# Kernel optimization log

Hardware: AMD Instinct MI355X
Metric: run time of the kernel (lower is better)

The kernel has to match this reference:

```python
import jax, jax.numpy as jnp
import numpy as np

NI = 512
POSE_DIM = 128
IMG_SEQ = 1024
ATTN_CHANS = 64
NHEADS = NI // ATTN_CHANS  # 8
SCALE = float(np.sqrt(NI / NHEADS))  # sqrt(64) = 8
EPS = 1e-5


def _layernorm(x, g, b):
    m = jnp.mean(x, axis=-1, keepdims=True)
    v = jnp.var(x, axis=-1, keepdims=True)
    return (x - m) * jax.lax.rsqrt(v + EPS) * g + b


def setup_inputs() -> dict:
    key = jax.random.key(0)
    ks = jax.random.split(key, 8)
    w = lambda k, shape: (jax.random.normal(k, shape, dtype=jnp.float32) * 0.02)
    return {
        "x": jax.random.normal(ks[0], (8, NI, 32, 32), dtype=jnp.float32),
        "pose_embed": jax.random.normal(ks[1], (8, 2, POSE_DIM), dtype=jnp.float32),
        "norm_g": jnp.ones((NI,), jnp.float32),
        "norm_b": jnp.zeros((NI,), jnp.float32),
        "pnorm_g": jnp.ones((NI + 2,), jnp.float32),
        "pnorm_b": jnp.zeros((NI + 2,), jnp.float32),
        "pose_W": w(ks[2], (POSE_DIM, IMG_SEQ)),
        "pose_b": jnp.zeros((IMG_SEQ,), jnp.float32),
        "q_W": w(ks[3], (NI, NI)),
        "q_b": jnp.zeros((NI,), jnp.float32),
        "k_W": w(ks[4], (NI + 2, NI)),
        "k_b": jnp.zeros((NI,), jnp.float32),
        "v_W": w(ks[5], (NI + 2, NI)),
        "v_b": jnp.zeros((NI,), jnp.float32),
        "proj_W": w(ks[6], (NI, NI)),
        "proj_b": jnp.zeros((NI,), jnp.float32),
    }


def reference(x, pose_embed, norm_g, norm_b, pnorm_g, pnorm_b, pose_W, pose_b,
              q_W, q_b, k_W, k_b, v_W, v_b, proj_W, proj_b):
    n, c, h, w = x.shape
    s = h * w  # == IMG_SEQ
    xs = x.reshape(n, c, s).transpose(0, 2, 1)              # (n, s, c)
    pe = pose_embed @ pose_W + pose_b                        # (n, 2, s)
    pe = pe.transpose(0, 2, 1)                               # (n, s, 2)
    x_pose = jnp.concatenate([xs, pe], axis=2)               # (n, s, c+2)
    xn = _layernorm(xs, norm_g, norm_b)
    xpn = _layernorm(x_pose, pnorm_g, pnorm_b)
    q = xn @ q_W + q_b                                       # (n, s, c)
    k = xpn @ k_W + k_b
    v = xpn @ v_W + v_b
    # faithful to original: concat along feature dim, THEN split heads, THEN chunk
    qkv = jnp.concatenate([q, k, v], axis=-1)                # (n, s, 3c)
    qkv = qkv.reshape(n, s, NHEADS, 3 * ATTN_CHANS).transpose(0, 2, 1, 3)  # (n, H, s, 3d)
    q2 = qkv[..., :ATTN_CHANS]
    k2 = qkv[..., ATTN_CHANS:2 * ATTN_CHANS]
    v2 = qkv[..., 2 * ATTN_CHANS:]
    att = jnp.einsum('nhsd,nhtd->nhst', q2, k2) / SCALE      # (n, H, s, s)
    p = jax.nn.softmax(att, axis=-1)
    o = jnp.einsum('nhst,nhtd->nhsd', p, v2)                 # (n, H, s, d)
    o = o.transpose(0, 2, 1, 3).reshape(n, s, c)             # (n, s, c)
    o = o @ proj_W + proj_b
    o = o.transpose(0, 2, 1)                                 # (n, c, s)
    return o.reshape(n, c, h, w)
```

## Files before the change

### kernel.cpp

```cpp
#include <hip/hip_runtime.h>
#include <hip/hip_bf16.h>

typedef unsigned short u16;
typedef unsigned int u32;
typedef unsigned long long u64;
typedef __attribute__((ext_vector_type(8))) short short8;
typedef __attribute__((ext_vector_type(4))) short short4v;
typedef __attribute__((ext_vector_type(4))) float f32x4;

__device__ __forceinline__ u16 f2bf(float f) {
    union { float f; u32 u; } x; x.f = f;
    u32 r = x.u + 0x7fffu + ((x.u >> 16) & 1u);
    return (u16)(r >> 16);
}
__device__ __forceinline__ u32 pkbf(float a, float b) {
    union { __hip_bfloat16 h; u16 u; } xa, xb;
    xa.h = __float2bfloat16(a);
    xb.h = __float2bfloat16(b);
    return (u32)xa.u | ((u32)xb.u << 16);
}
__device__ __forceinline__ float fast_exp2(float x) {
#if __has_builtin(__builtin_amdgcn_exp2f)
    return __builtin_amdgcn_exp2f(x);
#else
    return exp2f(x);
#endif
}
__device__ __forceinline__ f32x4 mfma16(short4v a, short4v b, f32x4 c) {
#if __has_builtin(__builtin_amdgcn_mfma_f32_16x16x16bf16_1k)
    return __builtin_amdgcn_mfma_f32_16x16x16bf16_1k(a, b, c, 0, 0, 0);
#else
    asm("v_mfma_f32_16x16x16_bf16 %0, %1, %2, %0" : "+v"(c) : "v"(a), "v"(b));
    return c;
#endif
}

#define AS1C const __attribute__((address_space(1))) void*
#define AS3  __attribute__((address_space(3))) void*

__global__ __launch_bounds__(256) void pe_kernel(
    const float* __restrict__ pose, const float* __restrict__ poseW,
    const float* __restrict__ poseB, float* __restrict__ out)
{
    __shared__ float pr[128];
    int bj = blockIdx.x, tid = threadIdx.x;
    if (tid < 128) pr[tid] = pose[bj * 128 + tid];
    __syncthreads();
#pragma unroll
    for (int r = 0; r < 4; ++r) {
        int t = r * 256 + tid;
        float acc = poseB[t];
        for (int p = 0; p < 128; ++p)
            acc += pr[p] * poseW[p * 1024 + t];
        out[bj * 1024 + t] = acc;
    }
}

__global__ __launch_bounds__(512) void lnpack_kernel(
    const float* __restrict__ x, const float* __restrict__ pe,
    const float* __restrict__ ng, const float* __restrict__ nb,
    const float* __restrict__ pg, const float* __restrict__ pb,
    u16* __restrict__ xn, u16* __restrict__ xpn)
{
    __shared__ float tile[512 * 33];
    __shared__ float red[2][32][17];
    __shared__ float stats[6][32];
    int tid = threadIdx.x;
    int b = blockIdx.y, t0 = blockIdx.x * 32;
#pragma unroll
    for (int it = 0; it < 8; ++it) {
        int ch = it * 512 + tid;
        int c = ch >> 3, tc = (ch & 7) * 4;
        const float* gp = x + ((size_t)b * 512 + c) * 1024 + t0 + tc;
        float4 v = *(const float4*)gp;
        float* rowp = tile + c * 33 + tc;
        rowp[0] = v.x; rowp[1] = v.y; rowp[2] = v.z; rowp[3] = v.w;
    }
    __syncthreads();
    {
        int tl = tid & 31, cg = tid >> 5;
        float s = 0.f, sq = 0.f;
        for (int i = 0; i < 32; ++i) {
            int c = cg * 32 + i;
            float v = tile[c * 33 + tl];
            s += v; sq += v * v;
        }
        red[0][tl][cg] = s; red[1][tl][cg] = sq;
    }
    __syncthreads();
    if (tid < 32) {
        float S = 0.f, Q = 0.f;
        for (int g = 0; g < 16; ++g) { S += red[0][tid][g]; Q += red[1][tid][g]; }
        float m1 = S * (1.f / 512.f);
        float v1 = fmaxf(Q * (1.f / 512.f) - m1 * m1, 0.f);
        float r1 = rsqrtf(v1 + 1e-5f);
        float p0 = pe[(size_t)b * 2048 + t0 + tid];
        float p1 = pe[(size_t)b * 2048 + 1024 + t0 + tid];
        float S2 = S + p0 + p1, Q2 = Q + p0 * p0 + p1 * p1;
        float m2 = S2 * (1.f / 514.f);
        float v2 = fmaxf(Q2 * (1.f / 514.f) - m2 * m2, 0.f);
        float r2 = rsqrtf(v2 + 1e-5f);
        stats[0][tid] = m1; stats[1][tid] = r1; stats[2][tid] = m2;
        stats[3][tid] = r2; stats[4][tid] = p0; stats[5][tid] = p1;
    }
    __syncthreads();
    {
        int c = tid;
        float g1 = ng[c], b1 = nb[c];
        float g2 = pg[c], b2 = pb[c];
        for (int t = 0; t < 32; ++t) {
            float v = tile[c * 33 + t];
            int T = t0 + t;
            xn [((size_t)b * 1024 + T) * 512 + c] = f2bf((v - stats[0][t]) * stats[1][t] * g1 + b1);
            xpn[((size_t)b * 1024 + T) * 544 + c] = f2bf((v - stats[2][t]) * stats[3][t] * g2 + b2);
        }
        if (tid < 32) {
            float gg = (tid < 2) ? pg[512 + tid] : 0.f;
            float bbv = (tid < 2) ? pb[512 + tid] : 0.f;
            for (int t = 0; t < 32; ++t) {
                float val = 0.f;
                if (tid < 2)
                    val = (stats[4 + tid][t] - stats[2][t]) * stats[3][t] * gg + bbv;
                xpn[((size_t)b * 1024 + (t0 + t)) * 544 + 512 + tid] = f2bf(val);
            }
        }
    }
}

__global__ __launch_bounds__(256) void wtrans_kernel(
    const float* __restrict__ qW, const float* __restrict__ kW,
    const float* __restrict__ vW, const float* __restrict__ pW,
    u16* __restrict__ qWt, u16* __restrict__ kWt,
    u16* __restrict__ vWt, u16* __restrict__ pWt)
{
    int z = blockIdx.z;
    const float* src = (z == 0) ? qW : (z == 1) ? kW : (z == 2) ? vW : pW;
    u16* dst = (z == 0) ? qWt : (z == 1) ? kWt : (z == 2) ? vWt : pWt;
    int Kdim = (z == 1 || z == 2) ? 514 : 512;
    int Kpad = (z == 1 || z == 2) ? 544 : 512;
    int n0 = blockIdx.x * 32, k0 = blockIdx.y * 32;
    if (k0 >= Kpad) return;
    __shared__ float tt[32][33];
    int xx = threadIdx.x & 31, yy = threadIdx.x >> 5;
#pragma unroll
    for (int r = 0; r < 4; ++r) {
        int k = k0 + yy * 4 + r;
        tt[xx][yy * 4 + r] = (k < Kdim) ? src[(size_t)k * 512 + n0 + xx] : 0.f;
    }
    __syncthreads();
#pragma unroll
    for (int r = 0; r < 4; ++r) {
        int nl = yy * 4 + r;
        dst[(size_t)(n0 + nl) * Kpad + k0 + xx] = f2bf(tt[nl][xx]);
    }
}

#define BM 128
#define BN 64
#define QSCALE 0.18033688f
__global__ __launch_bounds__(256) void gemm_kernel(
    const u16* __restrict__ A, int lda,
    const u16* __restrict__ Bt, int ldb,
    const float* __restrict__ bias0, const float* __restrict__ bias1,
    int K, int mode, int coff,
    u16* __restrict__ oq, u16* __restrict__ ok, u16* __restrict__ ov,
    float* __restrict__ out32)
{
    __shared__ __align__(16) u16 As[BM * 64];
    __shared__ __align__(16) u16 Bs[BN * 64];
    const int tid = threadIdx.x;
    const int lane = tid & 63, w = tid >> 6;
    const int row0 = blockIdx.x * BM, col0 = blockIdx.y * BN;
    const int woffM = (w & 1) * 64, woffN = (w >> 1) * 32;
    const int lr = lane & 15, kg = lane >> 4;
    f32x4 acc[4][2] = {};
    int k0 = 0;
    for (; k0 + 64 <= K; k0 += 64) {
#pragma unroll
        for (int h = 0; h < 6; ++h) {
            int c = tid + h * 256;
            if (c < 1024) {
                int r = c >> 3, sl = c & 7;
                int kc = sl ^ (r & 7);
                __builtin_amdgcn_global_load_lds(
                    (AS1C)(A + (size_t)(row0 + r) * lda + k0 + kc * 8),
                    (AS3)(As + c * 8), 16, 0, 0);
            } else {
                int cB = c - 1024;
                int r = cB >> 3, sl = cB & 7;
                int kc = sl ^ (r & 7);
                __builtin_amdgcn_global_load_lds(
                    (AS1C)(Bt + (size_t)(col0 + r) * ldb + k0 + kc * 8),
                    (AS3)(Bs + cB * 8), 16, 0, 0);
            }
        }
        __syncthreads();
        short8 af[4][2], bfr[2][2];
#pragma unroll
        for (int m = 0; m < 4; ++m) {
            int r = woffM + m * 16 + lr;
            const u16* base = As + r * 64;
            af[m][0] = *(const short8*)(base + ((kg ^ (r & 7)) * 8));
            af[m][1] = *(const short8*)(base + (((kg + 4) ^ (r & 7)) * 8));
        }
#pragma unroll
        for (int n = 0; n < 2; ++n) {
            int r = woffN + n * 16 + lr;
            const u16* base = Bs + r * 64;
            bfr[n][0] = *(const short8*)(base + ((kg ^ (r & 7)) * 8));
            bfr[n][1] = *(const short8*)(base + (((kg + 4) ^ (r & 7)) * 8));
        }
#pragma unroll
        for (int m = 0; m < 4; ++m)
#pragma unroll
            for (int n = 0; n < 2; ++n) {
                acc[m][n] = __builtin_amdgcn_mfma_f32_16x16x32_bf16(af[m][0], bfr[n][0], acc[m][n], 0, 0, 0);
                acc[m][n] = __builtin_amdgcn_mfma_f32_16x16x32_bf16(af[m][1], bfr[n][1], acc[m][n], 0, 0, 0);
            }
        __syncthreads();
    }
    if (k0 < K) {
#pragma unroll
        for (int h = 0; h < 3; ++h) {
            int c = tid + h * 256;
            if (c < 512) {
                int r = c >> 2, sl = c & 3;
                int kc = sl ^ (r & 3);
                __builtin_amdgcn_global_load_lds(
                    (AS1C)(A + (size_t)(row0 + r) * lda + k0 + kc * 8),
                    (AS3)(As + c * 8), 16, 0, 0);
            } else {
                int cB = c - 512;
                int r = cB >> 2, sl = cB & 3;
                int kc = sl ^ (r & 3);
                __builtin_amdgcn_global_load_lds(
                    (AS1C)(Bt + (size_t)(col0 + r) * ldb + k0 + kc * 8),
                    (AS3)(Bs + cB * 8), 16, 0, 0);
            }
        }
        __syncthreads();
        short8 af[4], bfr[2];
#pragma unroll
        for (int m = 0; m < 4; ++m) {
            int r = woffM + m * 16 + lr;
            af[m] = *(const short8*)(As + r * 32 + ((kg ^ (r & 3)) * 8));
        }
#pragma unroll
        for (int n = 0; n < 2; ++n) {
            int r = woffN + n * 16 + lr;
            bfr[n] = *(const short8*)(Bs + r * 32 + ((kg ^ (r & 3)) * 8));
        }
#pragma unroll
        for (int m = 0; m < 4; ++m)
#pragma unroll
            for (int n = 0; n < 2; ++n)
                acc[m][n] = __builtin_amdgcn_mfma_f32_16x16x32_bf16(af[m], bfr[n], acc[m][n], 0, 0, 0);
        __syncthreads();
    }
#pragma unroll
    for (int m = 0; m < 4; ++m) {
#pragma unroll
        for (int n = 0; n < 2; ++n) {
            int gcol = col0 + woffN + n * 16 + lr;
            float bv = (gcol < 512) ? bias0[gcol] : bias1[gcol - 512];
            int growb = row0 + woffM + m * 16 + kg * 4;
            int bb = growb >> 10, t0v = growb & 1023;
            float v0 = acc[m][n][0] + bv, v1 = acc[m][n][1] + bv;
            float v2 = acc[m][n][2] + bv, v3 = acc[m][n][3] + bv;
            if (mode == 0) {
                int cg = coff + gcol;
                int h = cg / 192;
                int rr = cg - h * 192;
                int role = rr >> 6, d = rr & 63;
                if (role == 0) { v0 *= QSCALE; v1 *= QSCALE; v2 *= QSCALE; v3 *= QSCALE; }
                if (role == 2) {
                    size_t base = ((((size_t)bb * 8 + h) * 64 + d) << 10) + t0v;
                    u64 pk = (u64)f2bf(v0) | ((u64)f2bf(v1) << 16)
                           | ((u64)f2bf(v2) << 32) | ((u64)f2bf(v3) << 48);
                    *(u64*)(ov + base) = pk;
                } else {
                    u16* o = role ? ok : oq;
                    size_t base = ((((size_t)bb * 8 + h) * 1024 + t0v) << 6) + d;
                    o[base]       = f2bf(v0);
                    o[base + 64]  = f2bf(v1);
                    o[base + 128] = f2bf(v2);
                    o[base + 192] = f2bf(v3);
                }
            } else {
                size_t base = (((size_t)bb * 512 + gcol) << 10) + t0v;
                float4 f4; f4.x = v0; f4.y = v1; f4.z = v2; f4.w = v3;
                *(float4*)(out32 + base) = f4;
            }
        }
    }
}

__global__ __launch_bounds__(256, 1) void attn_kernel(
    const u16* __restrict__ qb, const u16* __restrict__ kb,
    const u16* __restrict__ vt, u16* __restrict__ ob)
{
    __shared__ __align__(16) u16 Kl[2][4096];
    __shared__ __align__(16) u16 Vl[2][4096];
    int tid = threadIdx.x, lane = tid & 63, w = tid >> 6;
    int bid = blockIdx.x;
    int wid = (bid & 7) * 128 + (bid >> 3);
    int qt = wid & 15;
    int hh = (wid >> 4) & 7;
    int bbb = wid >> 7;
    int bh = bbb * 8 + hh;
    int q0 = qt * 64 + w * 16;
    int lr = lane & 15, kg = lane >> 4;
    const u16* qbase = qb + ((size_t)bh * 1024 + q0 + lr) * 64;
    short8 qf0 = *(const short8*)(qbase + kg * 8);
    short8 qf1 = *(const short8*)(qbase + 32 + kg * 8);
    f32x4 oT[4] = {};
    float lsum = 0.f;
    const u16* kbase = kb + (size_t)bh * 1024 * 64;
    const u16* vbase = vt + (size_t)bh * 64 * 1024;
    const int xr = lr & 7;
    const int vho = (kg & 1) * 4;
    const int vkg2 = kg >> 1;

#define STAGE(bf, s0) { \
    int g0 = tid, g1 = tid + 256; \
    { int r = g0 >> 3, cl = g0 & 7, cg = cl ^ (r & 7); \
      __builtin_amdgcn_global_load_lds((AS1C)(kbase + (size_t)((s0) + r) * 64 + cg * 8), \
                                       (AS3)(&Kl[bf][g0 * 8]), 16, 0, 0); } \
    { int r = g1 >> 3, cl = g1 & 7, cg = cl ^ (r & 7); \
      __builtin_amdgcn_global_load_lds((AS1C)(kbase + (size_t)((s0) + r) * 64 + cg * 8), \
                                       (AS3)(&Kl[bf][g1 * 8]), 16, 0, 0); } \
    { int d = g0 >> 3, cl = g0 & 7, cg = cl ^ (d & 7); \
      __builtin_amdgcn_global_load_lds((AS1C)(vbase + (size_t)d * 1024 + (s0) + cg * 8), \
                                       (AS3)(&Vl[bf][g0 * 8]), 16, 0, 0); } \
    { int d = g1 >> 3, cl = g1 & 7, cg = cl ^ (d & 7); \
      __builtin_amdgcn_global_load_lds((AS1C)(vbase + (size_t)d * 1024 + (s0) + cg * 8), \
                                       (AS3)(&Vl[bf][g1 * 8]), 16, 0, 0); } }

#define BODY(bf, st2) { \
    const u16* Kb = &Kl[bf][0]; \
    const u16* Vb = &Vl[bf][0]; \
    int rA = ((st2) * 32 + lr) * 64, rB = ((st2) * 32 + 16 + lr) * 64; \
    short8 k00 = *(const short8*)(Kb + rA + ((kg ^ xr) * 8)); \
    short8 k01 = *(const short8*)(Kb + rA + (((kg + 4) ^ xr) * 8)); \
    short8 k10 = *(const short8*)(Kb + rB + ((kg ^ xr) * 8)); \
    short8 k11 = *(const short8*)(Kb + rB + (((kg + 4) ^ xr) * 8)); \
    f32x4 sc0 = {}, sc1 = {}; \
    sc0 = __builtin_amdgcn_mfma_f32_16x16x32_bf16(k00, qf0, sc0, 0, 0, 0); \
    sc0 = __builtin_amdgcn_mfma_f32_16x16x32_bf16(k01, qf1, sc0, 0, 0, 0); \
    sc1 = __builtin_amdgcn_mfma_f32_16x16x32_bf16(k10, qf0, sc1, 0, 0, 0); \
    sc1 = __builtin_amdgcn_mfma_f32_16x16x32_bf16(k11, qf1, sc1, 0, 0, 0); \
    float p0 = fast_exp2(sc0[0]), p1 = fast_exp2(sc0[1]); \
    float p2 = fast_exp2(sc0[2]), p3 = fast_exp2(sc0[3]); \
    float p4 = fast_exp2(sc1[0]), p5 = fast_exp2(sc1[1]); \
    float p6 = fast_exp2(sc1[2]), p7 = fast_exp2(sc1[3]); \
    lsum += (((p0 + p1) + (p2 + p3)) + ((p4 + p5) + (p6 + p7))); \
    union { short4v s4; u32 u[2]; } pb0u, pb1u; \
    pb0u.u[0] = pkbf(p0, p1);  pb0u.u[1] = pkbf(p2, p3); \
    pb1u.u[0] = pkbf(p4, p5);  pb1u.u[1] = pkbf(p6, p7); \
    int c0 = ((((st2) * 4 + vkg2) ^ xr) * 8) + vho; \
    int c1 = ((((st2) * 4 + 2 + vkg2) ^ xr) * 8) + vho; \
    short4v va; \
    va = *(const short4v*)(Vb + (lr) * 64 + c0);       oT[0] = mfma16(va, pb0u.s4, oT[0]); \
    va = *(const short4v*)(Vb + (lr) * 64 + c1);       oT[0] = mfma16(va, pb1u.s4, oT[0]); \
    va = *(const short4v*)(Vb + (16 + lr) * 64 + c0);  oT[1] = mfma16(va, pb0u.s4, oT[1]); \
    va = *(const short4v*)(Vb + (16 + lr) * 64 + c1);  oT[1] = mfma16(va, pb1u.s4, oT[1]); \
    va = *(const short4v*)(Vb + (32 + lr) * 64 + c0);  oT[2] = mfma16(va, pb0u.s4, oT[2]); \
    va = *(const short4v*)(Vb + (32 + lr) * 64 + c1);  oT[2] = mfma16(va, pb1u.s4, oT[2]); \
    va = *(const short4v*)(Vb + (48 + lr) * 64 + c0);  oT[3] = mfma16(va, pb0u.s4, oT[3]); \
    va = *(const short4v*)(Vb + (48 + lr) * 64 + c1);  oT[3] = mfma16(va, pb1u.s4, oT[3]); }

    STAGE(0, 0)
    __syncthreads();
    for (int step = 0; step < 16; ++step) {
        int cur = step & 1;
        if (step < 15) STAGE(cur ^ 1, (step + 1) * 64)
        BODY(cur, 0)
        BODY(cur, 1)
        __syncthreads();
    }
#undef STAGE
#undef BODY

    float Z = lsum;
    Z += __shfl_xor(Z, 16);
    Z += __shfl_xor(Z, 32);
    float inv = 1.f / Z;
    u16* obase = ob + ((size_t)bbb * 1024 + q0 + lr) * 512 + hh * 64;
#pragma unroll
    for (int dt = 0; dt < 4; ++dt) {
        u32 lo = pkbf(oT[dt][0] * inv, oT[dt][1] * inv);
        u32 hi = pkbf(oT[dt][2] * inv, oT[dt][3] * inv);
        u32* dstp = (u32*)(obase + dt * 16 + kg * 4);
        dstp[0] = lo; dstp[1] = hi;
    }
}

extern "C" void kernel_launch(void* const* d_in, const int* in_sizes, int n_in,
                              void* d_out, int out_size, void* d_ws, size_t ws_size,
                              hipStream_t stream)
{
    (void)in_sizes; (void)n_in; (void)out_size;
    const float* x       = (const float*)d_in[0];
    const float* pose    = (const float*)d_in[1];
    const float* norm_g  = (const float*)d_in[2];
    const float* norm_b  = (const float*)d_in[3];
    const float* pnorm_g = (const float*)d_in[4];
    const float* pnorm_b = (const float*)d_in[5];
    const float* pose_W  = (const float*)d_in[6];
    const float* pose_b  = (const float*)d_in[7];
    const float* q_W     = (const float*)d_in[8];
    const float* q_b     = (const float*)d_in[9];
    const float* k_W     = (const float*)d_in[10];
    const float* k_b     = (const float*)d_in[11];
    const float* v_W     = (const float*)d_in[12];
    const float* v_b     = (const float*)d_in[13];
    const float* proj_W  = (const float*)d_in[14];
    const float* proj_b  = (const float*)d_in[15];
    float* out = (float*)d_out;

    if (ws_size < 44695552u) return;

    char* ws = (char*)d_ws;
    float* pe_ws = (float*)(ws);
    u16* xn    = (u16*)(ws + 65536);
    u16* xpn   = (u16*)(ws + 8454144);
    u16* qWt   = (u16*)(ws + 17367040);
    u16* kWt   = (u16*)(ws + 17891328);
    u16* vWt   = (u16*)(ws + 18448384);
    u16* pWt   = (u16*)(ws + 19005440);
    u16* qbuf  = (u16*)(ws + 19529728);
    u16* kbuf  = (u16*)(ws + 27918336);
    u16* vtb   = (u16*)(ws + 36306944);
    u16* obuf  = xn;

    hipLaunchKernelGGL(wtrans_kernel, dim3(16, 17, 4), dim3(256), 0, stream,
                       q_W, k_W, v_W, proj_W, qWt, kWt, vWt, pWt);
    hipLaunchKernelGGL(pe_kernel, dim3(16), dim3(256), 0, stream,
                       pose, pose_W, pose_b, pe_ws);
    hipLaunchKernelGGL(lnpack_kernel, dim3(32, 8), dim3(512), 0, stream,
                       x, pe_ws, norm_g, norm_b, pnorm_g, pnorm_b, xn, xpn);
    hipLaunchKernelGGL(gemm_kernel, dim3(64, 8), dim3(256), 0, stream,
                       xn, 512, qWt, 512, q_b, q_b, 512, 0, 0,
                       qbuf, kbuf, vtb, (float*)nullptr);
    hipLaunchKernelGGL(gemm_kernel, dim3(64, 16), dim3(256), 0, stream,
                       xpn, 544, kWt, 544, k_b, v_b, 544, 0, 512,
                       qbuf, kbuf, vtb, (float*)nullptr);
    hipLaunchKernelGGL(attn_kernel, dim3(1024), dim3(256), 0, stream,
                       qbuf, kbuf, vtb, obuf);
    hipLaunchKernelGGL(gemm_kernel, dim3(64, 8), dim3(256), 0, stream,
                       obuf, 512, pWt, 512, proj_b, proj_b, 512, 2, 0,
                       (u16*)nullptr, (u16*)nullptr, (u16*)nullptr, out);
}
```

Before: 111.1 us.

## Split attention work per wave into 32 queries by half the key tile

```diff
diff --git a/kernel.cpp b/kernel.cpp
--- a/kernel.cpp
+++ b/kernel.cpp
@@ -301,6 +301,7 @@
 {
     __shared__ __align__(16) u16 Kl[2][4096];
     __shared__ __align__(16) u16 Vl[2][4096];
+    __shared__ float zst[2][2][16];
     int tid = threadIdx.x, lane = tid & 63, w = tid >> 6;
     int bid = blockIdx.x;
     int wid = (bid & 7) * 128 + (bid >> 3);
@@ -308,18 +309,28 @@
     int hh = (wid >> 4) & 7;
     int bbb = wid >> 7;
     int bh = bbb * 8 + hh;
-    int q0 = qt * 64 + w * 16;
+    int q0 = qt * 64;
     int lr = lane & 15, kg = lane >> 4;
-    const u16* qbase = qb + ((size_t)bh * 1024 + q0 + lr) * 64;
-    short8 qf0 = *(const short8*)(qbase + kg * 8);
-    short8 qf1 = *(const short8*)(qbase + 32 + kg * 8);
-    f32x4 oT[4] = {};
-    float lsum = 0.f;
+    const int qp = w & 1;
+    const int sh = w >> 1;
+    const u16* qbase = qb + ((size_t)bh * 1024 + q0 + qp * 32 + lr) * 64;
+    short8 qA0 = *(const short8*)(qbase + kg * 8);
+    short8 qA1 = *(const short8*)(qbase + 32 + kg * 8);
+    short8 qB0 = *(const short8*)(qbase + 16 * 64 + kg * 8);
+    short8 qB1 = *(const short8*)(qbase + 16 * 64 + 32 + kg * 8);
+    f32x4 oT[2][4] = {};
+    float ls0 = 0.f, ls1 = 0.f;
     const u16* kbase = kb + (size_t)bh * 1024 * 64;
     const u16* vbase = vt + (size_t)bh * 64 * 1024;
     const int xr = lr & 7;
     const int vho = (kg & 1) * 4;
-    const int vkg2 = kg >> 1;
+    const int vk2 = kg >> 1;
+    const int krow0 = (sh * 32 + lr) * 64;
+    const int krow1 = (sh * 32 + 16 + lr) * 64;
+    const int kslotL = (kg ^ xr) * 8;
+    const int kslotH = ((kg + 4) ^ xr) * 8;
+    const int vc0 = ((sh * 4 + vk2) ^ xr) * 8 + vho;
+    const int vc1 = ((sh * 4 + 2 + vk2) ^ xr) * 8 + vho;
 
 #define STAGE(bf, s0) { \
     int g0 = tid, g1 = tid + 256; \
@@ -336,62 +347,92 @@
       __builtin_amdgcn_global_load_lds((AS1C)(vbase + (size_t)d * 1024 + (s0) + cg * 8), \
                                        (AS3)(&Vl[bf][g1 * 8]), 16, 0, 0); } }
 
-#define BODY(bf, st2) { \
+#define BODY(bf) { \
     const u16* Kb = &Kl[bf][0]; \
     const u16* Vb = &Vl[bf][0]; \
-    int rA = ((st2) * 32 + lr) * 64, rB = ((st2) * 32 + 16 + lr) * 64; \
-    short8 k00 = *(const short8*)(Kb + rA + ((kg ^ xr) * 8)); \
-    short8 k01 = *(const short8*)(Kb + rA + (((kg + 4) ^ xr) * 8)); \
-    short8 k10 = *(const short8*)(Kb + rB + ((kg ^ xr) * 8)); \
-    short8 k11 = *(const short8*)(Kb + rB + (((kg + 4) ^ xr) * 8)); \
-    f32x4 sc0 = {}, sc1 = {}; \
-    sc0 = __builtin_amdgcn_mfma_f32_16x16x32_bf16(k00, qf0, sc0, 0, 0, 0); \
-    sc0 = __builtin_amdgcn_mfma_f32_16x16x32_bf16(k01, qf1, sc0, 0, 0, 0); \
-    sc1 = __builtin_amdgcn_mfma_f32_16x16x32_bf16(k10, qf0, sc1, 0, 0, 0); \
-    sc1 = __builtin_amdgcn_mfma_f32_16x16x32_bf16(k11, qf1, sc1, 0, 0, 0); \
-    float p0 = fast_exp2(sc0[0]), p1 = fast_exp2(sc0[1]); \
-    float p2 = fast_exp2(sc0[2]), p3 = fast_exp2(sc0[3]); \
-    float p4 = fast_exp2(sc1[0]), p5 = fast_exp2(sc1[1]); \
-    float p6 = fast_exp2(sc1[2]), p7 = fast_exp2(sc1[3]); \
-    lsum += (((p0 + p1) + (p2 + p3)) + ((p4 + p5) + (p6 + p7))); \
-    union { short4v s4; u32 u[2]; } pb0u, pb1u; \
-    pb0u.u[0] = pkbf(p0, p1);  pb0u.u[1] = pkbf(p2, p3); \
-    pb1u.u[0] = pkbf(p4, p5);  pb1u.u[1] = pkbf(p6, p7); \
-    int c0 = ((((st2) * 4 + vkg2) ^ xr) * 8) + vho; \
-    int c1 = ((((st2) * 4 + 2 + vkg2) ^ xr) * 8) + vho; \
-    short4v va; \
-    va = *(const short4v*)(Vb + (lr) * 64 + c0);       oT[0] = mfma16(va, pb0u.s4, oT[0]); \
-    va = *(const short4v*)(Vb + (lr) * 64 + c1);       oT[0] = mfma16(va, pb1u.s4, oT[0]); \
-    va = *(const short4v*)(Vb + (16 + lr) * 64 + c0);  oT[1] = mfma16(va, pb0u.s4, oT[1]); \
-    va = *(const short4v*)(Vb + (16 + lr) * 64 + c1);  oT[1] = mfma16(va, pb1u.s4, oT[1]); \
-    va = *(const short4v*)(Vb + (32 + lr) * 64 + c0);  oT[2] = mfma16(va, pb0u.s4, oT[2]); \
-    va = *(const short4v*)(Vb + (32 + lr) * 64 + c1);  oT[2] = mfma16(va, pb1u.s4, oT[2]); \
-    va = *(const short4v*)(Vb + (48 + lr) * 64 + c0);  oT[3] = mfma16(va, pb0u.s4, oT[3]); \
-    va = *(const short4v*)(Vb + (48 + lr) * 64 + c1);  oT[3] = mfma16(va, pb1u.s4, oT[3]); }
+    short8 kL0 = *(const short8*)(Kb + krow0 + kslotL); \
+    short8 kH0 = *(const short8*)(Kb + krow0 + kslotH); \
+    short8 kL1 = *(const short8*)(Kb + krow1 + kslotL); \
+    short8 kH1 = *(const short8*)(Kb + krow1 + kslotH); \
+    f32x4 s00 = {}, s01 = {}, s10 = {}, s11 = {};   \
+    s00 = __builtin_amdgcn_mfma_f32_16x16x32_bf16(kL0, qA0, s00, 0, 0, 0); \
+    s00 = __builtin_amdgcn_mfma_f32_16x16x32_bf16(kH0, qA1, s00, 0, 0, 0); \
+    s01 = __builtin_amdgcn_mfma_f32_16x16x32_bf16(kL1, qA0, s01, 0, 0, 0); \
+    s01 = __builtin_amdgcn_mfma_f32_16x16x32_bf16(kH1, qA1, s01, 0, 0, 0); \
+    s10 = __builtin_amdgcn_mfma_f32_16x16x32_bf16(kL0, qB0, s10, 0, 0, 0); \
+    s10 = __builtin_amdgcn_mfma_f32_16x16x32_bf16(kH0, qB1, s10, 0, 0, 0); \
+    s11 = __builtin_amdgcn_mfma_f32_16x16x32_bf16(kL1, qB0, s11, 0, 0, 0); \
+    s11 = __builtin_amdgcn_mfma_f32_16x16x32_bf16(kH1, qB1, s11, 0, 0, 0); \
+    float a0 = fast_exp2(s00[0]), a1 = fast_exp2(s00[1]); \
+    float a2 = fast_exp2(s00[2]), a3 = fast_exp2(s00[3]); \
+    float a4 = fast_exp2(s01[0]), a5 = fast_exp2(s01[1]); \
+    float a6 = fast_exp2(s01[2]), a7 = fast_exp2(s01[3]); \
+    float b0 = fast_exp2(s10[0]), b1 = fast_exp2(s10[1]); \
+    float b2 = fast_exp2(s10[2]), b3 = fast_exp2(s10[3]); \
+    float b4 = fast_exp2(s11[0]), b5 = fast_exp2(s11[1]); \
+    float b6 = fast_exp2(s11[2]), b7 = fast_exp2(s11[3]); \
+    ls0 += (((a0 + a1) + (a2 + a3)) + ((a4 + a5) + (a6 + a7))); \
+    ls1 += (((b0 + b1) + (b2 + b3)) + ((b4 + b5) + (b6 + b7))); \
+    union { short4v s4; u32 u[2]; } pA0, pA1, pB0, pB1; \
+    pA0.u[0] = pkbf(a0, a1);  pA0.u[1] = pkbf(a2, a3); \
+    pA1.u[0] = pkbf(a4, a5);  pA1.u[1] = pkbf(a6, a7); \
+    pB0.u[0] = pkbf(b0, b1);  pB0.u[1] = pkbf(b2, b3); \
+    pB1.u[0] = pkbf(b4, b5);  pB1.u[1] = pkbf(b6, b7); \
+    _Pragma("unroll") \
+    for (int dt = 0; dt < 4; ++dt) { \
+        const u16* vrow = Vb + (dt * 16 + lr) * 64; \
+        short4v va0 = *(const short4v*)(vrow + vc0); \
+        short4v va1 = *(const short4v*)(vrow + vc1); \
+        oT[0][dt] = mfma16(va0, pA0.s4, oT[0][dt]); \
+        oT[0][dt] = mfma16(va1, pA1.s4, oT[0][dt]); \
+        oT[1][dt] = mfma16(va0, pB0.s4, oT[1][dt]); \
+        oT[1][dt] = mfma16(va1, pB1.s4, oT[1][dt]); \
+    } }
 
     STAGE(0, 0)
     __syncthreads();
     for (int step = 0; step < 16; ++step) {
         int cur = step & 1;
         if (step < 15) STAGE(cur ^ 1, (step + 1) * 64)
-        BODY(cur, 0)
-        BODY(cur, 1)
+        BODY(cur)
         __syncthreads();
     }
 #undef STAGE
 #undef BODY
 
-    float Z = lsum;
-    Z += __shfl_xor(Z, 16);
-    Z += __shfl_xor(Z, 32);
-    float inv = 1.f / Z;
-    u16* obase = ob + ((size_t)bbb * 1024 + q0 + lr) * 512 + hh * 64;
-#pragma unroll
-    for (int dt = 0; dt < 4; ++dt) {
-        u32 lo = pkbf(oT[dt][0] * inv, oT[dt][1] * inv);
-        u32 hi = pkbf(oT[dt][2] * inv, oT[dt][3] * inv);
-        u32* dstp = (u32*)(obase + dt * 16 + kg * 4);
-        dstp[0] = lo; dstp[1] = hi;
+    ls0 += __shfl_xor(ls0, 16);  ls0 += __shfl_xor(ls0, 32);
+    ls1 += __shfl_xor(ls1, 16);  ls1 += __shfl_xor(ls1, 32);
+    float* pbuf = (float*)&Kl[0][0];
+    if (w >= 2) {
+        if (lane < 16) { zst[qp][0][lane] = ls0; zst[qp][1][lane] = ls1; }
+        float* dst = pbuf + (w - 2) * 2048 + lane * 4;
+#pragma unroll
+        for (int j2 = 0; j2 < 2; ++j2)
+#pragma unroll
+            for (int dt = 0; dt < 4; ++dt)
+                *(f32x4*)(dst + (j2 * 4 + dt) * 256) = oT[j2][dt];
+    }
+    __syncthreads();
+    if (w < 2) {
+        const float* src = pbuf + w * 2048 + lane * 4;
+        float Z0 = ls0 + zst[qp][0][lr];
+        float Z1 = ls1 + zst[qp][1][lr];
+        float i0 = 1.f / Z0, i1 = 1.f / Z1;
+        u16* obase = ob + ((size_t)bbb * 1024 + q0 + qp * 32 + lr) * 512 + hh * 64;
+#pragma unroll
+        for (int j2 = 0; j2 < 2; ++j2) {
+            float iv = j2 ? i1 : i0;
+            u16* orow = obase + (size_t)j2 * 16 * 512;
+#pragma unroll
+            for (int dt = 0; dt < 4; ++dt) {
+                f32x4 p = *(const f32x4*)(src + (j2 * 4 + dt) * 256);
+                f32x4 s = oT[j2][dt];
+                u32 lo = pkbf((s[0] + p[0]) * iv, (s[1] + p[1]) * iv);
+                u32 hi = pkbf((s[2] + p[2]) * iv, (s[3] + p[3]) * iv);
+                u32* dstp = (u32*)(orow + dt * 16 + kg * 4);
+                dstp[0] = lo; dstp[1] = hi;
+            }
+        }
     }
 }
 
```

After: 111.2 us. No clear change (+0.1%).

## Split attention key range across wave pairs with 32-query tiles and LDS merge

Applied to the files above, without the earlier changes.

```diff
diff --git a/kernel.cpp b/kernel.cpp
--- a/kernel.cpp
+++ b/kernel.cpp
@@ -295,22 +295,25 @@
     }
 }
 
-__global__ __launch_bounds__(256, 1) void attn_kernel(
+__global__ __launch_bounds__(256, 8) void attn_kernel(
     const u16* __restrict__ qb, const u16* __restrict__ kb,
     const u16* __restrict__ vt, u16* __restrict__ ob)
 {
-    __shared__ __align__(16) u16 Kl[2][4096];
-    __shared__ __align__(16) u16 Vl[2][4096];
+    __shared__ __align__(16) u16 Kl[2][2048];
+    __shared__ __align__(16) u16 Vl[2][2048];
+    __shared__ float zst[2][16];
     int tid = threadIdx.x, lane = tid & 63, w = tid >> 6;
     int bid = blockIdx.x;
-    int wid = (bid & 7) * 128 + (bid >> 3);
-    int qt = wid & 15;
-    int hh = (wid >> 4) & 7;
-    int bbb = wid >> 7;
+    int wid = (bid & 7) * 256 + (bid >> 3);
+    int qt = wid & 31;
+    int hh = (wid >> 5) & 7;
+    int bbb = wid >> 8;
     int bh = bbb * 8 + hh;
-    int q0 = qt * 64 + w * 16;
+    int q0 = qt * 32;
     int lr = lane & 15, kg = lane >> 4;
-    const u16* qbase = qb + ((size_t)bh * 1024 + q0 + lr) * 64;
+    const int qp = w & 1;
+    const int sh = w >> 1;
+    const u16* qbase = qb + ((size_t)bh * 1024 + q0 + qp * 16 + lr) * 64;
     short8 qf0 = *(const short8*)(qbase + kg * 8);
     short8 qf1 = *(const short8*)(qbase + 32 + kg * 8);
     f32x4 oT[4] = {};
@@ -318,80 +321,76 @@
     const u16* kbase = kb + (size_t)bh * 1024 * 64;
     const u16* vbase = vt + (size_t)bh * 64 * 1024;
     const int xr = lr & 7;
+    const int krow = (sh * 16 + lr) * 64;
+    const int kslotL = (kg ^ xr) * 8;
+    const int kslotH = ((kg + 4) ^ xr) * 8;
+    const int vc4 = sh * 2 + (kg >> 1);
     const int vho = (kg & 1) * 4;
-    const int vkg2 = kg >> 1;
 
 #define STAGE(bf, s0) { \
-    int g0 = tid, g1 = tid + 256; \
-    { int r = g0 >> 3, cl = g0 & 7, cg = cl ^ (r & 7); \
+    { int r = tid >> 3, cl = tid & 7, cg = cl ^ (r & 7); \
       __builtin_amdgcn_global_load_lds((AS1C)(kbase + (size_t)((s0) + r) * 64 + cg * 8), \
-                                       (AS3)(&Kl[bf][g0 * 8]), 16, 0, 0); } \
-    { int r = g1 >> 3, cl = g1 & 7, cg = cl ^ (r & 7); \
-      __builtin_amdgcn_global_load_lds((AS1C)(kbase + (size_t)((s0) + r) * 64 + cg * 8), \
-                                       (AS3)(&Kl[bf][g1 * 8]), 16, 0, 0); } \
-    { int d = g0 >> 3, cl = g0 & 7, cg = cl ^ (d & 7); \
+                                       (AS3)(&Kl[bf][tid * 8]), 16, 0, 0); } \
+    { int d = tid >> 2, cl = tid & 3, cg = cl ^ (d & 3); \
       __builtin_amdgcn_global_load_lds((AS1C)(vbase + (size_t)d * 1024 + (s0) + cg * 8), \
-                                       (AS3)(&Vl[bf][g0 * 8]), 16, 0, 0); } \
-    { int d = g1 >> 3, cl = g1 & 7, cg = cl ^ (d & 7); \
-      __builtin_amdgcn_global_load_lds((AS1C)(vbase + (size_t)d * 1024 + (s0) + cg * 8), \
-                                       (AS3)(&Vl[bf][g1 * 8]), 16, 0, 0); } }
-
-#define BODY(bf, st2) { \
+                                       (AS3)(&Vl[bf][tid * 8]), 16, 0, 0); } }
+
+#define BODY(bf) { \
     const u16* Kb = &Kl[bf][0]; \
     const u16* Vb = &Vl[bf][0]; \
-    int rA = ((st2) * 32 + lr) * 64, rB = ((st2) * 32 + 16 + lr) * 64; \
-    short8 k00 = *(const short8*)(Kb + rA + ((kg ^ xr) * 8)); \
-    short8 k01 = *(const short8*)(Kb + rA + (((kg + 4) ^ xr) * 8)); \
-    short8 k10 = *(const short8*)(Kb + rB + ((kg ^ xr) * 8)); \
-    short8 k11 = *(const short8*)(Kb + rB + (((kg + 4) ^ xr) * 8)); \
-    f32x4 sc0 = {}, sc1 = {}; \
-    sc0 = __builtin_amdgcn_mfma_f32_16x16x32_bf16(k00, qf0, sc0, 0, 0, 0); \
-    sc0 = __builtin_amdgcn_mfma_f32_16x16x32_bf16(k01, qf1, sc0, 0, 0, 0); \
-    sc1 = __builtin_amdgcn_mfma_f32_16x16x32_bf16(k10, qf0, sc1, 0, 0, 0); \
-    sc1 = __builtin_amdgcn_mfma_f32_16x16x32_bf16(k11, qf1, sc1, 0, 0, 0); \
-    float p0 = fast_exp2(sc0[0]), p1 = fast_exp2(sc0[1]); \
-    float p2 = fast_exp2(sc0[2]), p3 = fast_exp2(sc0[3]); \
-    float p4 = fast_exp2(sc1[0]), p5 = fast_exp2(sc1[1]); \
-    float p6 = fast_exp2(sc1[2]), p7 = fast_exp2(sc1[3]); \
-    lsum += (((p0 + p1) + (p2 + p3)) + ((p4 + p5) + (p6 + p7))); \
-    union { short4v s4; u32 u[2]; } pb0u, pb1u; \
-    pb0u.u[0] = pkbf(p0, p1);  pb0u.u[1] = pkbf(p2, p3); \
-    pb1u.u[0] = pkbf(p4, p5);  pb1u.u[1] = pkbf(p6, p7); \
-    int c0 = ((((st2) * 4 + vkg2) ^ xr) * 8) + vho; \
-    int c1 = ((((st2) * 4 + 2 + vkg2) ^ xr) * 8) + vho; \
-    short4v va; \
-    va = *(const short4v*)(Vb + (lr) * 64 + c0);       oT[0] = mfma16(va, pb0u.s4, oT[0]); \
-    va = *(const short4v*)(Vb + (lr) * 64 + c1);       oT[0] = mfma16(va, pb1u.s4, oT[0]); \
-    va = *(const short4v*)(Vb + (16 + lr) * 64 + c0);  oT[1] = mfma16(va, pb0u.s4, oT[1]); \
-    va = *(const short4v*)(Vb + (16 + lr) * 64 + c1);  oT[1] = mfma16(va, pb1u.s4, oT[1]); \
-    va = *(const short4v*)(Vb + (32 + lr) * 64 + c0);  oT[2] = mfma16(va, pb0u.s4, oT[2]); \
-    va = *(const short4v*)(Vb + (32 + lr) * 64 + c1);  oT[2] = mfma16(va, pb1u.s4, oT[2]); \
-    va = *(const short4v*)(Vb + (48 + lr) * 64 + c0);  oT[3] = mfma16(va, pb0u.s4, oT[3]); \
-    va = *(const short4v*)(Vb + (48 + lr) * 64 + c1);  oT[3] = mfma16(va, pb1u.s4, oT[3]); }
+    short8 kL = *(const short8*)(Kb + krow + kslotL); \
+    short8 kH = *(const short8*)(Kb + krow + kslotH); \
+    f32x4 sc = {}; \
+    sc = __builtin_amdgcn_mfma_f32_16x16x32_bf16(kL, qf0, sc, 0, 0, 0); \
+    sc = __builtin_amdgcn_mfma_f32_16x16x32_bf16(kH, qf1, sc, 0, 0, 0); \
+    float p0 = fast_exp2(sc[0]), p1 = fast_exp2(sc[1]); \
+    float p2 = fast_exp2(sc[2]), p3 = fast_exp2(sc[3]); \
+    lsum += ((p0 + p1) + (p2 + p3)); \
+    union { short4v s4; u32 u[2]; } pb; \
+    pb.u[0] = pkbf(p0, p1);  pb.u[1] = pkbf(p2, p3); \
+    _Pragma("unroll") \
+    for (int dt = 0; dt < 4; ++dt) { \
+        int dr = dt * 16 + lr; \
+        short4v va = *(const short4v*)(Vb + dr * 32 + ((vc4 ^ (dr & 3)) * 8) + vho); \
+        oT[dt] = mfma16(va, pb.s4, oT[dt]); \
+    } }
 
     STAGE(0, 0)
     __syncthreads();
-    for (int step = 0; step < 16; ++step) {
+    for (int step = 0; step < 32; ++step) {
         int cur = step & 1;
-        if (step < 15) STAGE(cur ^ 1, (step + 1) * 64)
-        BODY(cur, 0)
-        BODY(cur, 1)
+        if (step < 31) STAGE(cur ^ 1, (step + 1) * 32)
+        BODY(cur)
         __syncthreads();
     }
 #undef STAGE
 #undef BODY
 
-    float Z = lsum;
-    Z += __shfl_xor(Z, 16);
-    Z += __shfl_xor(Z, 32);
-    float inv = 1.f / Z;
-    u16* obase = ob + ((size_t)bbb * 1024 + q0 + lr) * 512 + hh * 64;
-#pragma unroll
-    for (int dt = 0; dt < 4; ++dt) {
-        u32 lo = pkbf(oT[dt][0] * inv, oT[dt][1] * inv);
-        u32 hi = pkbf(oT[dt][2] * inv, oT[dt][3] * inv);
-        u32* dstp = (u32*)(obase + dt * 16 + kg * 4);
-        dstp[0] = lo; dstp[1] = hi;
+    lsum += __shfl_xor(lsum, 16);
+    lsum += __shfl_xor(lsum, 32);
+    float* pbuf = (float*)&Kl[0][0];
+    if (sh == 1) {
+        if (lane < 16) zst[qp][lane] = lsum;
+        float* dst = pbuf + qp * 1024 + lr * 64 + kg * 4;
+#pragma unroll
+        for (int dt = 0; dt < 4; ++dt)
+            *(f32x4*)(dst + dt * 16) = oT[dt];
+    }
+    __syncthreads();
+    if (sh == 0) {
+        const float* src = pbuf + qp * 1024 + lr * 64 + kg * 4;
+        float Z = lsum + zst[qp][lr];
+        float inv = 1.f / Z;
+        u16* obase = ob + ((size_t)bbb * 1024 + q0 + qp * 16 + lr) * 512 + hh * 64;
+#pragma unroll
+        for (int dt = 0; dt < 4; ++dt) {
+            f32x4 p = *(const f32x4*)(src + dt * 16);
+            f32x4 s = oT[dt];
+            u32 lo = pkbf((s[0] + p[0]) * inv, (s[1] + p[1]) * inv);
+            u32 hi = pkbf((s[2] + p[2]) * inv, (s[3] + p[3]) * inv);
+            u32* dstp = (u32*)(obase + dt * 16 + kg * 4);
+            dstp[0] = lo; dstp[1] = hi;
+        }
     }
 }
 
@@ -445,7 +444,7 @@
     hipLaunchKernelGGL(gemm_kernel, dim3(64, 16), dim3(256), 0, stream,
                        xpn, 544, kWt, 544, k_b, v_b, 544, 0, 512,
                        qbuf, kbuf, vtb, (float*)nullptr);
-    hipLaunchKernelGGL(attn_kernel, dim3(1024), dim3(256), 0, stream,
+    hipLaunchKernelGGL(attn_kernel, dim3(2048), dim3(256), 0, stream,
                        qbuf, kbuf, vtb, obuf);
     hipLaunchKernelGGL(gemm_kernel, dim3(64, 8), dim3(256), 0, stream,
                        obuf, 512, pWt, 512, proj_b, proj_b, 512, 2, 0,
```

New measurement: 121.5 us. +9.4%, slower.
